# Kernel tuning notes

Hardware: AMD Instinct MI355X
Metric: run time of the kernel (lower is better)

## Reference

```python
import jax, jax.numpy as jnp
import numpy as np

LOG2E = 1.4426950408889634  # log2(e), same constant as the Triton kernel
TEMPERATURE = 0.07
BLK = 1024  # row-block size for blockwise (flash-style) sum-exp accumulation


def setup_inputs() -> dict:
    key = jax.random.key(0)
    k1, k2 = jax.random.split(key)
    B, D = 8192, 512
    return {
        "image_features": jax.random.normal(k1, (B, D), dtype=jnp.float32),
        "text_features": jax.random.normal(k2, (B, D), dtype=jnp.float32),
    }


def reference(image_features, text_features):
    inv_temp = LOG2E / TEMPERATURE  # kernel's inv_temperature (base-2 units)
    # normalized_inputs=False -> L2-normalize along dim=1 (F.normalize)
    Xn = image_features / jnp.linalg.norm(image_features, axis=1, keepdims=True)
    Yn = text_features / jnp.linalg.norm(text_features, axis=1, keepdims=True)
    B = Xn.shape[0]

    # Blockwise accumulation of row/col sums of exp2(S*inv_temp - inv_temp),
    # never materializing the full BxB similarity matrix (mirrors clip_sum_exp_kernel).
    def step(col_sum, x_blk):
        # x_blk: [BLK, D]; E: [BLK, B]
        E = jnp.exp2(x_blk @ Yn.T * inv_temp - inv_temp)
        return col_sum + E.sum(axis=0), E.sum(axis=1)

    col_sum, row_blocks = jax.lax.scan(
        step, jnp.zeros(B, dtype=jnp.float32), Xn.reshape(B // BLK, BLK, -1)
    )
    row_sum = row_blocks.reshape(B)

    # Diagonal (positive-pair) logits, in base-2 units exactly as the source:
    # Sv = <x_i, y_i> * inv_temp - inv_temp
    Sv = jnp.sum(Xn * Yn, axis=-1) * inv_temp - inv_temp
    # Faithful to source: logits = log(exp(Sv)/row_sum) + log(exp(Sv)/col_sum)
    # (note: source uses natural exp on base-2-scaled Sv; log(exp(Sv)/s) == Sv - log(s))
    logits = (Sv - jnp.log(row_sum)) + (Sv - jnp.log(col_sum))
    loss = -jnp.mean(logits) / 2.0
    return loss
```

## Files before the change

kernel.cpp:

```cpp
#include <hip/hip_runtime.h>

#define NB 8192
#define DD 512
#define INV_T 20.609929155556618f

typedef short bf16x8 __attribute__((ext_vector_type(8)));
typedef float f32x4  __attribute__((ext_vector_type(4)));

__device__ static inline unsigned short f2bf(float f) {
  unsigned int u = __float_as_uint(f);
  u += 0x7fff + ((u >> 16) & 1);
  return (unsigned short)(u >> 16);
}

__device__ static inline void async16(const void* lds, const void* g) {
  __builtin_amdgcn_global_load_lds(
      (const __attribute__((address_space(1))) unsigned int*)g,
      (__attribute__((address_space(3))) unsigned int*)lds, 16, 0, 0);
}

__global__ __launch_bounds__(256) void norm_kernel(
    const float* __restrict__ X, const float* __restrict__ Y,
    unsigned short* __restrict__ Xnb, unsigned short* __restrict__ Ynb,
    float* __restrict__ Sv) {
  const int wv   = threadIdx.x >> 6;
  const int lane = threadIdx.x & 63;
  const int row  = blockIdx.x * 4 + wv;
  const float4* x4 = (const float4*)(X + (size_t)row * DD);
  const float4* y4 = (const float4*)(Y + (size_t)row * DD);
  float4 xa = x4[lane * 2], xb = x4[lane * 2 + 1];
  float4 ya = y4[lane * 2], yb = y4[lane * 2 + 1];
  float xs[8] = {xa.x, xa.y, xa.z, xa.w, xb.x, xb.y, xb.z, xb.w};
  float ys[8] = {ya.x, ya.y, ya.z, ya.w, yb.x, yb.y, yb.z, yb.w};
  float ssx = 0.f, ssy = 0.f, sxy = 0.f;
#pragma unroll
  for (int k = 0; k < 8; ++k) {
    ssx += xs[k] * xs[k];
    ssy += ys[k] * ys[k];
    sxy += xs[k] * ys[k];
  }
#pragma unroll
  for (int m = 1; m < 64; m <<= 1) {
    ssx += __shfl_xor(ssx, m);
    ssy += __shfl_xor(ssy, m);
    sxy += __shfl_xor(sxy, m);
  }
  const float rnx = 1.0f / sqrtf(ssx);
  const float rny = 1.0f / sqrtf(ssy);
  unsigned short ox[8], oy[8];
#pragma unroll
  for (int k = 0; k < 8; ++k) {
    ox[k] = f2bf(xs[k] * rnx);
    oy[k] = f2bf(ys[k] * rny);
  }
  *(uint4*)(Xnb + (size_t)row * DD + lane * 8) = *(const uint4*)ox;
  *(uint4*)(Ynb + (size_t)row * DD + lane * 8) = *(const uint4*)oy;
  if (lane == 0) Sv[row] = sxy * rnx * rny * INV_T - INV_T;
}


#define STAGE_HALF(SRC, ROW0, LBASE, T) do {                                   \
  _Pragma("unroll") for (int s_ = 0; s_ < 2; ++s_) {                           \
    const int Pl_ = s_ * 8192 + tid * 16;                                      \
    const int L_  = Pl_ ^ (((Pl_ >> 7) & 7) << 4);                             \
    async16(sT + (LBASE) + s_ * 8192 + wv * 1024,                              \
            (const char*)(SRC) + (size_t)((ROW0) + (L_ >> 7)) * 1024           \
              + (T) * 128 + (L_ & 127));                                       \
  } } while (0)

#define STAGE_A(B_, T_) do {                                                   \
    STAGE_HALF(Xnb, br * 256,       (B_),         (T_));                       \
    STAGE_HALF(Xnb, br * 256 + 128, (B_) + 16384, (T_)); } while (0)
#define STAGE_B(B_, T_) do {                                                   \
    STAGE_HALF(Ynb, bc * 256,       (B_) + 32768, (T_));                       \
    STAGE_HALF(Ynb, bc * 256 + 128, (B_) + 49152, (T_)); } while (0)

#define READ_A(B_, MH) do {                                                    \
  _Pragma("unroll") for (int ks_ = 0; ks_ < 2; ++ks_)                          \
  _Pragma("unroll") for (int i_ = 0; i_ < 4; ++i_)                             \
    af[MH][ks_][i_] = *(const bf16x8*)(sT +                                    \
      (((B_) + aoffL + (MH) * 8192 + i_ * 2048 + ks_ * 64) ^ aswz));           \
  } while (0)

#define READ_B(B_, J0) do {                                                    \
  _Pragma("unroll") for (int ks_ = 0; ks_ < 2; ++ks_)                          \
  _Pragma("unroll") for (int j_ = 0; j_ < 2; ++j_)                             \
    bfr[ks_][(J0) + j_] = *(const bf16x8*)(sT +                                \
      (((B_) + boffL + ((J0) + j_) * 2048 + ks_ * 64) ^ aswz));                \
  } while (0)

#define QUAD(MH, NH) do {                                                      \
  __builtin_amdgcn_s_setprio(1);                                               \
  _Pragma("unroll") for (int ks_ = 0; ks_ < 2; ++ks_)                          \
  _Pragma("unroll") for (int i_ = 0; i_ < 4; ++i_)                             \
  _Pragma("unroll") for (int j_ = 0; j_ < 2; ++j_)                             \
    acc[(MH) * 4 + i_][(NH) * 2 + j_] =                                        \
      __builtin_amdgcn_mfma_f32_16x16x32_bf16(                                 \
        af[MH][ks_][i_], bfr[ks_][(NH) * 2 + j_],                              \
        acc[(MH) * 4 + i_][(NH) * 2 + j_], 0, 0, 0);                           \
  __builtin_amdgcn_s_setprio(0);                                               \
  } while (0)

__global__ __launch_bounds__(512, 1) void gemm_kernel(
    const unsigned short* __restrict__ Xnb, const unsigned short* __restrict__ Ynb,
    float* __restrict__ rowp, float* __restrict__ colp) {
  extern __shared__ __align__(16) char sT[];
  float* rp = (float*)(sT + 131072);
  float* cp = (float*)(sT + 131072 + 4096);

  const int tid  = threadIdx.x;
  const int wv   = tid >> 6;
  const int lane = tid & 63;
  const int l16  = lane & 15;
  const int lg   = lane >> 4;
  const int wr   = wv >> 2, wc = wv & 3;
  const int br   = blockIdx.y, bc = blockIdx.x;

  const int aswz  = (l16 & 7) << 4;
  const int aoffL = (wr * 128 + l16) * 128 + lg * 16;
  const int boffL = 32768 + (wc * 64 + l16) * 128 + lg * 16;

  f32x4  acc[8][4] = {};
  bf16x8 af[2][2][4];
  bf16x8 bfr[2][4];

  STAGE_A(0, 0);
  STAGE_B(0, 0);
  asm volatile("s_waitcnt vmcnt(0)" ::: "memory");
  __builtin_amdgcn_s_barrier();
  asm volatile("" ::: "memory");
  READ_A(0, 0);
  READ_B(0, 0);

  for (int t = 0; t < 8; ++t) {
    const int base  = (t & 1) << 16;
    const int other = base ^ (1 << 16);
    const bool pf   = (t < 7);
    READ_B(base, 2);
    if (pf) STAGE_A(other, t + 1);
    __builtin_amdgcn_s_barrier();
    QUAD(0, 0);
    __builtin_amdgcn_s_barrier();
    READ_A(base, 1);
    if (pf) STAGE_B(other, t + 1);
    __builtin_amdgcn_s_barrier();
    QUAD(0, 1);
    __builtin_amdgcn_s_barrier();
    QUAD(1, 0);
    if (pf) asm volatile("s_waitcnt vmcnt(0)" ::: "memory");
    asm volatile("s_barrier" ::: "memory");
    if (pf) {
      READ_A(other, 0);
      READ_B(other, 0);
    }
    QUAD(1, 1);
    __builtin_amdgcn_s_barrier();
  }

  float cacc[4] = {0.f, 0.f, 0.f, 0.f};
#pragma unroll
  for (int I = 0; I < 8; ++I) {
    float racc[4] = {0.f, 0.f, 0.f, 0.f};
#pragma unroll
    for (int J = 0; J < 4; ++J)
#pragma unroll
      for (int r = 0; r < 4; ++r) {
        const float e = exp2f(fmaf(acc[I][J][r], INV_T, -INV_T));
        racc[r] += e;
        cacc[J] += e;
      }
#pragma unroll
    for (int r = 0; r < 4; ++r) {
      float v = racc[r];
      v += __shfl_xor(v, 1); v += __shfl_xor(v, 2);
      v += __shfl_xor(v, 4); v += __shfl_xor(v, 8);
      if (l16 == 0) rp[wc * 256 + wr * 128 + I * 16 + lg * 4 + r] = v;
    }
  }
#pragma unroll
  for (int J = 0; J < 4; ++J) {
    float v = cacc[J];
    v += __shfl_xor(v, 16); v += __shfl_xor(v, 32);
    if (lg == 0) cp[wr * 256 + wc * 64 + J * 16 + l16] = v;
  }
  __syncthreads();
  if (tid < 256) {
    rowp[(size_t)bc * NB + br * 256 + tid] =
        rp[tid] + rp[256 + tid] + rp[512 + tid] + rp[768 + tid];
  } else {
    const int c = tid - 256;
    colp[(size_t)br * NB + bc * 256 + c] = cp[c] + cp[256 + c];
  }
}

__global__ __launch_bounds__(256) void loss_kernel(
    const float* __restrict__ rowp, const float* __restrict__ colp,
    const float* __restrict__ Sv, float* __restrict__ out) {
  __shared__ float wsum[4];
  const int i = blockIdx.x * 256 + threadIdx.x;
  float rs = 0.f, cs = 0.f;
  for (int b = 0; b < 32; ++b) {
    rs += rowp[(size_t)b * NB + i];
    cs += colp[(size_t)b * NB + i];
  }
  float v = 2.f * Sv[i] - logf(rs) - logf(cs);
#pragma unroll
  for (int m = 1; m < 64; m <<= 1) v += __shfl_xor(v, m);
  if ((threadIdx.x & 63) == 0) wsum[threadIdx.x >> 6] = v;
  __syncthreads();
  if (threadIdx.x == 0) {
    const float s = wsum[0] + wsum[1] + wsum[2] + wsum[3];
    atomicAdd(out, s * (-1.0f / (2.0f * NB)));
  }
}

extern "C" void kernel_launch(void* const* d_in, const int* in_sizes, int n_in,
                              void* d_out, int out_size, void* d_ws, size_t ws_size,
                              hipStream_t stream) {
  const float* X = (const float*)d_in[0];
  const float* Y = (const float*)d_in[1];
  char* ws = (char*)d_ws;
  unsigned short* Xnb = (unsigned short*)(ws);
  unsigned short* Ynb = (unsigned short*)(ws + 8388608);
  float* Sv   = (float*)(ws + 16777216);
  float* rowp = (float*)(ws + 16777216 + 32768);
  float* colp = (float*)(ws + 16777216 + 32768 + 1048576);
  float* out  = (float*)d_out;

  (void)hipFuncSetAttribute((const void*)gemm_kernel,
                            hipFuncAttributeMaxDynamicSharedMemorySize,
                            131072 + 6144);

  hipMemsetAsync(d_out, 0, sizeof(float), stream);
  norm_kernel<<<NB / 4, 256, 0, stream>>>(X, Y, Xnb, Ynb, Sv);
  gemm_kernel<<<dim3(32, 32), 512, 131072 + 6144, stream>>>(Xnb, Ynb, rowp, colp);
  loss_kernel<<<32, 256, 0, stream>>>(rowp, colp, Sv, out);
}
```

Before: 182.1 us.

## Remap GEMM tiles across XCDs, precompute LDS addressing, reorder pipeline, coalesce norm loads

The GEMM grid becomes 1D and each block index is remapped so that blocks on the same XCD share rows and columns, which should improve L2 reuse. Global staging offsets and swizzled LDS read addresses are now computed once per thread instead of every iteration. The last MFMA quad moves before the wait and barrier, and the reduction scratch reuses the tile LDS so total LDS shrinks. The norm kernel switches to fully coalesced float4 loads with split bf16 stores, and the loss loop is unrolled. The new pipeline order drops one barrier but places the stage wait after more compute, which changes how much global-load latency is hidden.

```diff
diff --git a/kernel.cpp b/kernel.cpp
--- a/kernel.cpp
+++ b/kernel.cpp
@@ -19,7 +19,7 @@
       (__attribute__((address_space(3))) unsigned int*)lds, 16, 0, 0);
 }
 
-__global__ __launch_bounds__(256) void norm_kernel(
+__global__ __launch_bounds__(256) void norm_kernel2(
     const float* __restrict__ X, const float* __restrict__ Y,
     unsigned short* __restrict__ Xnb, unsigned short* __restrict__ Ynb,
     float* __restrict__ Sv) {
@@ -28,8 +28,8 @@
   const int row  = blockIdx.x * 4 + wv;
   const float4* x4 = (const float4*)(X + (size_t)row * DD);
   const float4* y4 = (const float4*)(Y + (size_t)row * DD);
-  float4 xa = x4[lane * 2], xb = x4[lane * 2 + 1];
-  float4 ya = y4[lane * 2], yb = y4[lane * 2 + 1];
+  float4 xa = x4[lane], xb = x4[lane + 64];
+  float4 ya = y4[lane], yb = y4[lane + 64];
   float xs[8] = {xa.x, xa.y, xa.z, xa.w, xb.x, xb.y, xb.z, xb.w};
   float ys[8] = {ya.x, ya.y, ya.z, ya.w, yb.x, yb.y, yb.z, yb.w};
   float ssx = 0.f, ssy = 0.f, sxy = 0.f;
@@ -53,40 +53,42 @@
     ox[k] = f2bf(xs[k] * rnx);
     oy[k] = f2bf(ys[k] * rny);
   }
-  *(uint4*)(Xnb + (size_t)row * DD + lane * 8) = *(const uint4*)ox;
-  *(uint4*)(Ynb + (size_t)row * DD + lane * 8) = *(const uint4*)oy;
+  *(uint2*)(Xnb + (size_t)row * DD + lane * 4)       = *(const uint2*)&ox[0];
+  *(uint2*)(Xnb + (size_t)row * DD + 256 + lane * 4) = *(const uint2*)&ox[4];
+  *(uint2*)(Ynb + (size_t)row * DD + lane * 4)       = *(const uint2*)&oy[0];
+  *(uint2*)(Ynb + (size_t)row * DD + 256 + lane * 4) = *(const uint2*)&oy[4];
   if (lane == 0) Sv[row] = sxy * rnx * rny * INV_T - INV_T;
 }
 
 
-#define STAGE_HALF(SRC, ROW0, LBASE, T) do {                                   \
-  _Pragma("unroll") for (int s_ = 0; s_ < 2; ++s_) {                           \
-    const int Pl_ = s_ * 8192 + tid * 16;                                      \
-    const int L_  = Pl_ ^ (((Pl_ >> 7) & 7) << 4);                             \
-    async16(sT + (LBASE) + s_ * 8192 + wv * 1024,                              \
-            (const char*)(SRC) + (size_t)((ROW0) + (L_ >> 7)) * 1024           \
-              + (T) * 128 + (L_ & 127));                                       \
+#define STAGE_A(BUF, T) do {                                                   \
+  _Pragma("unroll") for (int h_ = 0; h_ < 2; ++h_) {                           \
+    async16(sT + (BUF) + h_ * 16384 + wv * 1024,                               \
+            Ab + h_ * 131072 + (T) * 128 + g0);                                \
+    async16(sT + (BUF) + h_ * 16384 + 8192 + wv * 1024,                        \
+            Ab + h_ * 131072 + (T) * 128 + g1);                                \
   } } while (0)
 
-#define STAGE_A(B_, T_) do {                                                   \
-    STAGE_HALF(Xnb, br * 256,       (B_),         (T_));                       \
-    STAGE_HALF(Xnb, br * 256 + 128, (B_) + 16384, (T_)); } while (0)
-#define STAGE_B(B_, T_) do {                                                   \
-    STAGE_HALF(Ynb, bc * 256,       (B_) + 32768, (T_));                       \
-    STAGE_HALF(Ynb, bc * 256 + 128, (B_) + 49152, (T_)); } while (0)
-
-#define READ_A(B_, MH) do {                                                    \
+#define STAGE_B(BUF, T) do {                                                   \
+  _Pragma("unroll") for (int h_ = 0; h_ < 2; ++h_) {                           \
+    async16(sT + (BUF) + 32768 + h_ * 16384 + wv * 1024,                       \
+            Bb + h_ * 131072 + (T) * 128 + g0);                                \
+    async16(sT + (BUF) + 32768 + h_ * 16384 + 8192 + wv * 1024,                \
+            Bb + h_ * 131072 + (T) * 128 + g1);                                \
+  } } while (0)
+
+#define READ_A(BUF, MH) do {                                                   \
   _Pragma("unroll") for (int ks_ = 0; ks_ < 2; ++ks_)                          \
   _Pragma("unroll") for (int i_ = 0; i_ < 4; ++i_)                             \
-    af[MH][ks_][i_] = *(const bf16x8*)(sT +                                    \
-      (((B_) + aoffL + (MH) * 8192 + i_ * 2048 + ks_ * 64) ^ aswz));           \
+    af[MH][ks_][i_] = *(const bf16x8*)(sT + (BUF) + raB[ks_]                   \
+                                       + (MH) * 8192 + i_ * 2048);             \
   } while (0)
 
-#define READ_B(B_, J0) do {                                                    \
+#define READ_B(BUF, J0) do {                                                   \
   _Pragma("unroll") for (int ks_ = 0; ks_ < 2; ++ks_)                          \
   _Pragma("unroll") for (int j_ = 0; j_ < 2; ++j_)                             \
-    bfr[ks_][(J0) + j_] = *(const bf16x8*)(sT +                                \
-      (((B_) + boffL + ((J0) + j_) * 2048 + ks_ * 64) ^ aswz));                \
+    bfr[ks_][(J0) + j_] = *(const bf16x8*)(sT + (BUF) + rbB[ks_]               \
+                                           + ((J0) + j_) * 2048);              \
   } while (0)
 
 #define QUAD(MH, NH) do {                                                      \
@@ -105,8 +107,6 @@
     const unsigned short* __restrict__ Xnb, const unsigned short* __restrict__ Ynb,
     float* __restrict__ rowp, float* __restrict__ colp) {
   extern __shared__ __align__(16) char sT[];
-  float* rp = (float*)(sT + 131072);
-  float* cp = (float*)(sT + 131072 + 4096);
 
   const int tid  = threadIdx.x;
   const int wv   = tid >> 6;
@@ -114,11 +114,28 @@
   const int l16  = lane & 15;
   const int lg   = lane >> 4;
   const int wr   = wv >> 2, wc = wv & 3;
-  const int br   = blockIdx.y, bc = blockIdx.x;
-
-  const int aswz  = (l16 & 7) << 4;
-  const int aoffL = (wr * 128 + l16) * 128 + lg * 16;
-  const int boffL = 32768 + (wc * 64 + l16) * 128 + lg * 16;
+
+  const int bid = blockIdx.x;
+  const int xcd = bid & 7;
+  const int idx = bid >> 3;
+  const int w   = idx & 31;
+  const int br  = (idx >> 5) * 8 + (w & 7);
+  const int bc  = xcd * 4 + (w >> 3);
+
+  const int Pl0 = tid * 16;
+  const int L0  = Pl0 ^ (((Pl0 >> 7) & 7) << 4);
+  const int Pl1 = 8192 + tid * 16;
+  const int L1  = Pl1 ^ (((Pl1 >> 7) & 7) << 4);
+  const int g0  = (L0 >> 7) * 1024 + (L0 & 127);
+  const int g1  = (L1 >> 7) * 1024 + (L1 & 127);
+  const char* Ab = (const char*)Xnb + (size_t)br * 262144;
+  const char* Bb = (const char*)Ynb + (size_t)bc * 262144;
+
+  const int aswz = (l16 & 7) << 4;
+  const int raB[2] = { (wr * 128 + l16) * 128 + ((lg * 16)      ^ aswz),
+                       (wr * 128 + l16) * 128 + ((lg * 16 + 64) ^ aswz) };
+  const int rbB[2] = { 32768 + (wc * 64 + l16) * 128 + ((lg * 16)      ^ aswz),
+                       32768 + (wc * 64 + l16) * 128 + ((lg * 16 + 64) ^ aswz) };
 
   f32x4  acc[8][4] = {};
   bf16x8 af[2][2][4];
@@ -147,16 +164,19 @@
     QUAD(0, 1);
     __builtin_amdgcn_s_barrier();
     QUAD(1, 0);
+    QUAD(1, 1);
     if (pf) asm volatile("s_waitcnt vmcnt(0)" ::: "memory");
-    asm volatile("s_barrier" ::: "memory");
+    __builtin_amdgcn_s_barrier();
+    asm volatile("" ::: "memory");
     if (pf) {
       READ_A(other, 0);
       READ_B(other, 0);
     }
-    QUAD(1, 1);
-    __builtin_amdgcn_s_barrier();
-  }
-
+  }
+
+  __syncthreads();
+  float* rp = (float*)sT;
+  float* cp = (float*)(sT + 4096);
   float cacc[4] = {0.f, 0.f, 0.f, 0.f};
 #pragma unroll
   for (int I = 0; I < 8; ++I) {
@@ -199,6 +219,7 @@
   __shared__ float wsum[4];
   const int i = blockIdx.x * 256 + threadIdx.x;
   float rs = 0.f, cs = 0.f;
+#pragma unroll 4
   for (int b = 0; b < 32; ++b) {
     rs += rowp[(size_t)b * NB + i];
     cs += colp[(size_t)b * NB + i];
@@ -229,10 +250,10 @@
 
   (void)hipFuncSetAttribute((const void*)gemm_kernel,
                             hipFuncAttributeMaxDynamicSharedMemorySize,
-                            131072 + 6144);
+                            131072);
 
   hipMemsetAsync(d_out, 0, sizeof(float), stream);
-  norm_kernel<<<NB / 4, 256, 0, stream>>>(X, Y, Xnb, Ynb, Sv);
-  gemm_kernel<<<dim3(32, 32), 512, 131072 + 6144, stream>>>(Xnb, Ynb, rowp, colp);
+  norm_kernel2<<<NB / 4, 256, 0, stream>>>(X, Y, Xnb, Ynb, Sv);
+  gemm_kernel<<<1024, 512, 131072, stream>>>(Xnb, Ynb, rowp, colp);
   loss_kernel<<<32, 256, 0, stream>>>(rowp, colp, Sv, out);
 }
```

After: 167.5 us. -8.0%, faster.
